# Optimization experiments

Measured on AMD Instinct MI355X. Metric: run time of the kernel, lower is better.

The kernel has to match this reference:

```python
import jax, jax.numpy as jnp
import numpy as np

M, K, E, N, TOPK = 4096, 1024, 8, 1024, 2

def setup_inputs() -> dict:
    key = jax.random.key(0)
    k1, k2, k3, k4, k5 = jax.random.split(key, 5)
    hidden_states = jax.random.normal(k1, (M, K), dtype=jnp.float32)
    w1 = jax.random.normal(k2, (E, K, 2 * N), dtype=jnp.float32) * 0.02
    w2 = jax.random.normal(k3, (E, N, K), dtype=jnp.float32) * 0.02
    topk_weights = jax.random.uniform(k4, (M, TOPK), dtype=jnp.float32)
    topk_ids = jax.random.randint(k5, (M, TOPK), 0, E, dtype=jnp.int64)
    return {"hidden_states": hidden_states, "w1": w1, "w2": w2,
            "topk_weights": topk_weights, "topk_ids": topk_ids}

def reference(hidden_states, w1, w2, topk_weights, topk_ids):
    # Fused MoE: per expert e, y_e = silu_and_mul(x @ w1[e]) @ w2[e];
    # output[m] = sum_k topk_weights[m,k] * y_{topk_ids[m,k]}[m]
    num_experts = w1.shape[0]
    n = w2.shape[1]

    def expert_step(acc, inputs):
        w1_e, w2_e, e = inputs
        gate_up = hidden_states @ w1_e            # [M, 2N]
        gate, up = gate_up[:, :n], gate_up[:, n:]
        h = jax.nn.silu(gate) * up                 # [M, N]
        y_e = h @ w2_e                             # [M, K]
        # combined routing weight of expert e per token (scatter-free finalize)
        coef = jnp.sum(jnp.where(topk_ids == e, topk_weights, 0.0), axis=1)  # [M]
        return acc + coef[:, None] * y_e, None

    init = jnp.zeros_like(hidden_states)
    out, _ = jax.lax.scan(expert_step, init,
                          (w1, w2, jnp.arange(num_experts, dtype=topk_ids.dtype)))
    return out
```

## Files before the change

kernel.cpp:

```cpp
#include <hip/hip_runtime.h>


#define M_TOK   4096
#define K_DIM   1024
#define N_DIM   1024
#define E_NUM   8
#define NPAIR   8192
#define BM      64
#define ROWS_CAP 8704
#define NROWBLK 136
#define HBLK    32

typedef unsigned short u16;
typedef unsigned int   u32;
typedef __attribute__((ext_vector_type(8))) short bf16x8;
typedef __attribute__((ext_vector_type(4))) float f32x4;

#define GPTR(p) ((const __attribute__((address_space(1))) u32*)(const void*)(p))
#define LPTR(p) ((__attribute__((address_space(3))) u32*)(void*)(p))

__device__ __forceinline__ u16 f2bf(float f) {
  union { float f; u32 u; } v; v.f = f;
  u32 r = v.u + 0x7FFFu + ((v.u >> 16) & 1u);
  return (u16)(r >> 16);
}
__device__ __forceinline__ float bf2f(u16 u) {
  union { u32 u; float f; } v; v.u = ((u32)u) << 16;
  return v.f;
}

__global__ __launch_bounds__(256) void hist_kernel(
    const int* __restrict__ topk_ids, int* __restrict__ blockhist) {
  __shared__ int wcnt[4][E_NUM];
  const int t = threadIdx.x, wave = t >> 6, lane = t & 63;
  int e = topk_ids[blockIdx.x * 256 + t] & 7;
#pragma unroll
  for (int ee = 0; ee < E_NUM; ++ee) {
    unsigned long long m = __ballot(e == ee);
    if (lane == ee) wcnt[wave][ee] = (int)__popcll(m);
  }
  __syncthreads();
  if (t < E_NUM) {
    int s = wcnt[0][t] + wcnt[1][t] + wcnt[2][t] + wcnt[3][t];
    blockhist[blockIdx.x * E_NUM + t] = s;
  }
}

__global__ __launch_bounds__(256) void scan_kernel(
    const int* __restrict__ blockhist, int* __restrict__ baseoff,
    int* __restrict__ pair_token, int* __restrict__ block_expert) {
  __shared__ int cnt[E_NUM], off[E_NUM], pad[E_NUM];
  const int t = threadIdx.x;
  if (t < E_NUM) {
    int run = 0;
    for (int b = 0; b < HBLK; ++b) {
      baseoff[b * E_NUM + t] = run;
      run += blockhist[b * E_NUM + t];
    }
    cnt[t] = run;
  }
  __syncthreads();
  if (t == 0) {
    int run = 0, blk = 0;
    for (int e = 0; e < E_NUM; ++e) {
      off[e] = run;
      int padded = ((cnt[e] + BM - 1) / BM) * BM;
      pad[e] = padded;
      for (int b = 0; b < padded / BM; ++b) block_expert[blk++] = e;
      run += padded;
    }
    for (; blk < NROWBLK; ++blk) block_expert[blk] = -1;
  }
  __syncthreads();
  for (int i = t; i < HBLK * E_NUM; i += 256) baseoff[i] += off[i & 7];
  for (int e = 0; e < E_NUM; ++e) {
    int s = off[e] + cnt[e], epos = off[e] + pad[e];
    for (int r = s + t; r < epos; r += 256) pair_token[r] = 0;
  }
}

__global__ __launch_bounds__(256) void assign_kernel(
    const int* __restrict__ topk_ids, const int* __restrict__ baseoff,
    int* __restrict__ pair_token, int* __restrict__ pos_of) {
  __shared__ int wcnt[4][E_NUM], wbase[4][E_NUM];
  const int t = threadIdx.x, wave = t >> 6, lane = t & 63;
  const int p = blockIdx.x * 256 + t;
  const int e = topk_ids[p] & 7;
  int rank = 0;
#pragma unroll
  for (int ee = 0; ee < E_NUM; ++ee) {
    unsigned long long m = __ballot(e == ee);
    if (e == ee) rank = (int)__popcll(m & ((1ull << lane) - 1ull));
    if (lane == ee) wcnt[wave][ee] = (int)__popcll(m);
  }
  __syncthreads();
  if (t < E_NUM) {
    int run = baseoff[blockIdx.x * E_NUM + t];
    for (int w = 0; w < 4; ++w) { wbase[w][t] = run; run += wcnt[w][t]; }
  }
  __syncthreads();
  int pos = wbase[wave][e] + rank;
  pair_token[pos] = p >> 1;
  pos_of[p] = pos;
}

__global__ __launch_bounds__(256) void convert_kernel(
    const float* __restrict__ in, u16* __restrict__ out) {
  int i = blockIdx.x * 256 + threadIdx.x;
  float4 v = ((const float4*)in)[i];
  ushort4 o;
  o.x = f2bf(v.x); o.y = f2bf(v.y); o.z = f2bf(v.z); o.w = f2bf(v.w);
  ((ushort4*)out)[i] = o;
}

__global__ __launch_bounds__(256) void transpose_convert(
    const float* __restrict__ in, u16* __restrict__ out, int R, int Cc) {
  __shared__ float lds[64][65];
  const float* src = in + (size_t)blockIdx.z * R * Cc;
  u16* dst = out + (size_t)blockIdx.z * R * Cc;
  int r0 = blockIdx.x * 64, c0 = blockIdx.y * 64;
  int t = threadIdx.x;
#pragma unroll
  for (int it = 0; it < 16; ++it) {
    int lin = it * 256 + t;
    int rr = lin >> 6, cc = lin & 63;
    lds[cc][rr] = src[(size_t)(r0 + rr) * Cc + c0 + cc];
  }
  __syncthreads();
#pragma unroll
  for (int it = 0; it < 8; ++it) {
    int lin = it * 512 + t * 2;
    int cc = lin >> 6, rr = lin & 63;
    ushort2 o;
    o.x = f2bf(lds[cc][rr]);
    o.y = f2bf(lds[cc][rr + 1]);
    *(ushort2*)&dst[(size_t)(c0 + cc) * R + r0 + rr] = o;
  }
}

template <bool GATHER, int NB>
__global__ __launch_bounds__(256, NB == 2 ? 3 : 4) void gemm64(
    const u16* __restrict__ A, const u16* __restrict__ Bt, u16* __restrict__ Out,
    const int* __restrict__ pair_token, const int* __restrict__ block_expert) {
  const int e = block_expert[blockIdx.x];
  if (e < 0) return;
  __shared__ __align__(16) u16 As[64 * 64];
  __shared__ __align__(16) u16 Bs[NB * 128 * 64];
  const int tid = threadIdx.x;
  const int wave = tid >> 6;
  const int lane = tid & 63;
  const int srow = wave * 8 + (lane >> 3);
  const int kc = ((lane & 7) ^ (srow & 7)) << 3;

  const u16* ap[2];
#pragma unroll
  for (int is = 0; is < 2; ++is) {
    int rt = is * 32 + srow;
    int grow = blockIdx.x * BM + rt;
    int arow = GATHER ? pair_token[grow] : grow;
    ap[is] = A + (size_t)arow * K_DIM + kc;
  }
  const u16* bp[NB][4];
  const u16* base_e = Bt + (size_t)e * (NB * N_DIM) * K_DIM;
#pragma unroll
  for (int nb = 0; nb < NB; ++nb)
#pragma unroll
    for (int is = 0; is < 4; ++is) {
      int rt = is * 32 + srow;
      int n = nb * N_DIM + blockIdx.y * 128 + rt;
      bp[nb][is] = base_e + (size_t)n * K_DIM + kc;
    }
  u16* alds = As + wave * 512;
  u16* blds = Bs + wave * 512;

  f32x4 acc[NB][4][2];
#pragma unroll
  for (int nb = 0; nb < NB; ++nb)
#pragma unroll
    for (int i = 0; i < 4; ++i)
#pragma unroll
      for (int j = 0; j < 2; ++j) acc[nb][i][j] = f32x4{0.f, 0.f, 0.f, 0.f};

  for (int k0 = 0; k0 < K_DIM; k0 += 64) {
#pragma unroll
    for (int is = 0; is < 2; ++is)
      __builtin_amdgcn_global_load_lds(GPTR(ap[is] + k0), LPTR(alds + is * 2048), 16, 0, 0);
#pragma unroll
    for (int nb = 0; nb < NB; ++nb)
#pragma unroll
      for (int is = 0; is < 4; ++is)
        __builtin_amdgcn_global_load_lds(GPTR(bp[nb][is] + k0), LPTR(blds + nb * 8192 + is * 2048), 16, 0, 0);
    __syncthreads();
#pragma unroll
    for (int ks = 0; ks < 2; ++ks) {
      const int cq = ks * 4 + (lane >> 4);
      bf16x8 af[4], bfr[NB][2];
#pragma unroll
      for (int i = 0; i < 4; ++i) {
        int row = i * 16 + (lane & 15);
        af[i] = *(const bf16x8*)&As[row * 64 + ((cq ^ (row & 7)) << 3)];
      }
#pragma unroll
      for (int nb = 0; nb < NB; ++nb)
#pragma unroll
        for (int j = 0; j < 2; ++j) {
          int n = wave * 32 + j * 16 + (lane & 15);
          bfr[nb][j] = *(const bf16x8*)&Bs[nb * 8192 + n * 64 + ((cq ^ (n & 7)) << 3)];
        }
#pragma unroll
      for (int nb = 0; nb < NB; ++nb)
#pragma unroll
        for (int i = 0; i < 4; ++i)
#pragma unroll
          for (int j = 0; j < 2; ++j)
            acc[nb][i][j] = __builtin_amdgcn_mfma_f32_16x16x32_bf16(af[i], bfr[nb][j], acc[nb][i][j], 0, 0, 0);
    }
    __syncthreads();
  }

  const size_t rbase = (size_t)blockIdx.x * BM + ((lane >> 4) * 4);
  const int cbase = blockIdx.y * 128 + wave * 32 + (lane & 15);
#pragma unroll
  for (int i = 0; i < 4; ++i)
#pragma unroll
    for (int j = 0; j < 2; ++j)
#pragma unroll
      for (int r = 0; r < 4; ++r) {
        float v;
        if (NB == 2) {
          float g = acc[0][i][j][r], u = acc[1][i][j][r];
          v = g * u / (1.f + __expf(-g));
        } else {
          v = acc[0][i][j][r];
        }
        Out[(rbase + i * 16 + r) * N_DIM + cbase + j * 16] = f2bf(v);
      }
}

__global__ __launch_bounds__(256) void gather_kernel(
    const u16* __restrict__ y, const float* __restrict__ tw,
    const int* __restrict__ pos_of, float* __restrict__ out) {
  int m = blockIdx.x;
  int k = threadIdx.x * 4;
  int p0 = pos_of[m * 2 + 0], p1 = pos_of[m * 2 + 1];
  float w0 = tw[m * 2 + 0], w1 = tw[m * 2 + 1];
  ushort4 y0 = *(const ushort4*)&y[(size_t)p0 * 1024 + k];
  ushort4 y1 = *(const ushort4*)&y[(size_t)p1 * 1024 + k];
  float4 o;
  o.x = w0 * bf2f(y0.x) + w1 * bf2f(y1.x);
  o.y = w0 * bf2f(y0.y) + w1 * bf2f(y1.y);
  o.z = w0 * bf2f(y0.z) + w1 * bf2f(y1.z);
  o.w = w0 * bf2f(y0.w) + w1 * bf2f(y1.w);
  *(float4*)&out[(size_t)m * 1024 + k] = o;
}

extern "C" void kernel_launch(void* const* d_in, const int* in_sizes, int n_in,
                              void* d_out, int out_size, void* d_ws, size_t ws_size,
                              hipStream_t stream) {
  const float* hs = (const float*)d_in[0];
  const float* w1 = (const float*)d_in[1];
  const float* w2 = (const float*)d_in[2];
  const float* tw = (const float*)d_in[3];
  const int* tids = (const int*)d_in[4];
  float* out = (float*)d_out;

  char* ws = (char*)d_ws;
  u16* hsb = (u16*)(ws);
  u16* w1t = (u16*)(ws + (size_t)(8u << 20));
  u16* w2t = (u16*)(ws + (size_t)(40u << 20));
  u16* h   = (u16*)(ws + (size_t)(56u << 20));
  u16* y   = (u16*)(ws + (size_t)(76u << 20));
  int* pair_token   = (int*)(ws + (size_t)(96u << 20));
  int* pos_of       = (int*)(ws + (size_t)(96u << 20) + 64 * 1024);
  int* block_expert = (int*)(ws + (size_t)(96u << 20) + 128 * 1024);
  int* blockhist    = (int*)(ws + (size_t)(96u << 20) + 192 * 1024);
  int* baseoff      = (int*)(ws + (size_t)(96u << 20) + 256 * 1024);

  hist_kernel<<<HBLK, 256, 0, stream>>>(tids, blockhist);
  scan_kernel<<<1, 256, 0, stream>>>(blockhist, baseoff, pair_token, block_expert);
  assign_kernel<<<HBLK, 256, 0, stream>>>(tids, baseoff, pair_token, pos_of);
  convert_kernel<<<4096, 256, 0, stream>>>(hs, hsb);
  transpose_convert<<<dim3(16, 32, E_NUM), 256, 0, stream>>>(w1, w1t, 1024, 2048);
  transpose_convert<<<dim3(16, 16, E_NUM), 256, 0, stream>>>(w2, w2t, 1024, 1024);
  gemm64<true, 2><<<dim3(NROWBLK, 8), 256, 0, stream>>>(hsb, w1t, h, pair_token, block_expert);
  gemm64<false, 1><<<dim3(NROWBLK, 8), 256, 0, stream>>>(h, w2t, y, pair_token, block_expert);
  gather_kernel<<<4096, 256, 0, stream>>>(y, tw, pos_of, out);
}
```

Before: 264.0 us.

## Fuse prep kernels and software-pipeline expert GEMMs with register-held B tiles

Merges the hidden-state conversion, both weight transpose-converts and the routing histogram into one launch to cut launch overhead and idle gaps. Rewrites the grouped GEMM as a double-buffered pipeline. A tiles stream into LDS via global_load_lds two steps ahead, while B fragments are loaded straight from global memory into registers and prefetched ahead, so B no longer goes through LDS. It also flattens the grid so the eight column blocks of one row block run adjacently, which should improve expert weight reuse in cache. The trade-off is higher register pressure (lower occupancy hints) and uncoalesced per-lane B loads.

```diff
diff --git a/kernel.cpp b/kernel.cpp
--- a/kernel.cpp
+++ b/kernel.cpp
@@ -10,6 +10,7 @@
 #define ROWS_CAP 8704
 #define NROWBLK 136
 #define HBLK    32
+#define NK      16
 
 typedef unsigned short u16;
 typedef unsigned int   u32;
@@ -29,20 +30,63 @@
   return v.f;
 }
 
-__global__ __launch_bounds__(256) void hist_kernel(
-    const int* __restrict__ topk_ids, int* __restrict__ blockhist) {
+__device__ __forceinline__ void transpose_body(
+    const float* __restrict__ in, u16* __restrict__ out, int R, int Cc,
+    int xt, int yt, int zt, float (*lds)[65]) {
+  const float* src = in + (size_t)zt * R * Cc;
+  u16* dst = out + (size_t)zt * R * Cc;
+  int r0 = xt * 64, c0 = yt * 64;
+  int t = threadIdx.x;
+#pragma unroll
+  for (int it = 0; it < 16; ++it) {
+    int lin = it * 256 + t;
+    int rr = lin >> 6, cc = lin & 63;
+    lds[cc][rr] = src[(size_t)(r0 + rr) * Cc + c0 + cc];
+  }
+  __syncthreads();
+#pragma unroll
+  for (int it = 0; it < 8; ++it) {
+    int lin = it * 512 + t * 2;
+    int cc = lin >> 6, rr = lin & 63;
+    ushort2 o;
+    o.x = f2bf(lds[cc][rr]);
+    o.y = f2bf(lds[cc][rr + 1]);
+    *(ushort2*)&dst[(size_t)(c0 + cc) * R + r0 + rr] = o;
+  }
+}
+
+__global__ __launch_bounds__(256) void prep_kernel(
+    const float* __restrict__ hs, const float* __restrict__ w1,
+    const float* __restrict__ w2, const int* __restrict__ topk_ids,
+    u16* __restrict__ hsb, u16* __restrict__ w1t, u16* __restrict__ w2t,
+    int* __restrict__ blockhist) {
+  __shared__ float tlds[64][65];
   __shared__ int wcnt[4][E_NUM];
-  const int t = threadIdx.x, wave = t >> 6, lane = t & 63;
-  int e = topk_ids[blockIdx.x * 256 + t] & 7;
-#pragma unroll
-  for (int ee = 0; ee < E_NUM; ++ee) {
-    unsigned long long m = __ballot(e == ee);
-    if (lane == ee) wcnt[wave][ee] = (int)__popcll(m);
-  }
-  __syncthreads();
-  if (t < E_NUM) {
-    int s = wcnt[0][t] + wcnt[1][t] + wcnt[2][t] + wcnt[3][t];
-    blockhist[blockIdx.x * E_NUM + t] = s;
+  const int b = blockIdx.x, t = threadIdx.x;
+  if (b < 4096) {
+    int i = b * 256 + t;
+    float4 v = ((const float4*)hs)[i];
+    ushort4 o;
+    o.x = f2bf(v.x); o.y = f2bf(v.y); o.z = f2bf(v.z); o.w = f2bf(v.w);
+    ((ushort4*)hsb)[i] = o;
+  } else if (b < 8192) {
+    int idx = b - 4096;
+    transpose_body(w1, w1t, 1024, 2048, idx & 15, (idx >> 4) & 31, idx >> 9, tlds);
+  } else if (b < 10240) {
+    int idx = b - 8192;
+    transpose_body(w2, w2t, 1024, 1024, idx & 15, (idx >> 4) & 15, idx >> 8, tlds);
+  } else {
+    int blk = b - 10240;
+    const int wave = t >> 6, lane = t & 63;
+    int e = topk_ids[blk * 256 + t] & 7;
+#pragma unroll
+    for (int ee = 0; ee < E_NUM; ++ee) {
+      unsigned long long m = __ballot(e == ee);
+      if (lane == ee) wcnt[wave][ee] = (int)__popcll(m);
+    }
+    __syncthreads();
+    if (t < E_NUM)
+      blockhist[blk * E_NUM + t] = wcnt[0][t] + wcnt[1][t] + wcnt[2][t] + wcnt[3][t];
   }
 }
 
@@ -104,48 +148,46 @@
   pos_of[p] = pos;
 }
 
-__global__ __launch_bounds__(256) void convert_kernel(
-    const float* __restrict__ in, u16* __restrict__ out) {
-  int i = blockIdx.x * 256 + threadIdx.x;
-  float4 v = ((const float4*)in)[i];
-  ushort4 o;
-  o.x = f2bf(v.x); o.y = f2bf(v.y); o.z = f2bf(v.z); o.w = f2bf(v.w);
-  ((ushort4*)out)[i] = o;
-}
-
-__global__ __launch_bounds__(256) void transpose_convert(
-    const float* __restrict__ in, u16* __restrict__ out, int R, int Cc) {
-  __shared__ float lds[64][65];
-  const float* src = in + (size_t)blockIdx.z * R * Cc;
-  u16* dst = out + (size_t)blockIdx.z * R * Cc;
-  int r0 = blockIdx.x * 64, c0 = blockIdx.y * 64;
-  int t = threadIdx.x;
-#pragma unroll
-  for (int it = 0; it < 16; ++it) {
-    int lin = it * 256 + t;
-    int rr = lin >> 6, cc = lin & 63;
-    lds[cc][rr] = src[(size_t)(r0 + rr) * Cc + c0 + cc];
-  }
-  __syncthreads();
-#pragma unroll
-  for (int it = 0; it < 8; ++it) {
-    int lin = it * 512 + t * 2;
-    int cc = lin >> 6, rr = lin & 63;
-    ushort2 o;
-    o.x = f2bf(lds[cc][rr]);
-    o.y = f2bf(lds[cc][rr + 1]);
-    *(ushort2*)&dst[(size_t)(c0 + cc) * R + r0 + rr] = o;
-  }
-}
-
-template <bool GATHER, int NB>
-__global__ __launch_bounds__(256, NB == 2 ? 3 : 4) void gemm64(
+#define STEP(it, cur)                                                          \
+  {                                                                            \
+    bf16x8 afr[2][4];                                                          \
+    _Pragma("unroll") for (int ks = 0; ks < 2; ++ks)                           \
+      _Pragma("unroll") for (int i = 0; i < 4; ++i) {                          \
+        int row = i * 16 + (lane & 15);                                        \
+        int cq = ks * 4 + (lane >> 4);                                         \
+        afr[ks][i] = *(const bf16x8*)&As[(cur) * 4096 + row * 64 +             \
+                                         ((cq ^ (row & 7)) << 3)];             \
+      }                                                                        \
+    __syncthreads();                                                           \
+    if ((it) + 2 < NK) {                                                       \
+      _Pragma("unroll") for (int is = 0; is < 2; ++is)                         \
+        __builtin_amdgcn_global_load_lds(GPTR(ap[is] + (it) * 64 + 128),       \
+            LPTR(As + (cur) * 4096 + wave * 512 + is * 2048), 16, 0, 0);       \
+    }                                                                          \
+    _Pragma("unroll") for (int ks = 0; ks < 2; ++ks)                           \
+      _Pragma("unroll") for (int nb = 0; nb < NB; ++nb)                        \
+        _Pragma("unroll") for (int i = 0; i < 4; ++i)                          \
+          _Pragma("unroll") for (int j = 0; j < 2; ++j)                        \
+            acc[nb][i][j] = __builtin_amdgcn_mfma_f32_16x16x32_bf16(           \
+                afr[ks][i], breg[cur][nb][j][ks], acc[nb][i][j], 0, 0, 0);     \
+    if ((it) + 2 < NK) {                                                       \
+      _Pragma("unroll") for (int nb = 0; nb < NB; ++nb)                        \
+        _Pragma("unroll") for (int j = 0; j < 2; ++j)                          \
+          _Pragma("unroll") for (int ks = 0; ks < 2; ++ks)                     \
+            breg[cur][nb][j][ks] =                                             \
+                *(const bf16x8*)(bq[nb][j] + (it) * 64 + 128 + ks * 32);       \
+    }                                                                          \
+  }
+
+template <bool GATHER, int NB, int MINW>
+__global__ __launch_bounds__(256, MINW) void gemm_pl(
     const u16* __restrict__ A, const u16* __restrict__ Bt, u16* __restrict__ Out,
     const int* __restrict__ pair_token, const int* __restrict__ block_expert) {
-  const int e = block_expert[blockIdx.x];
+  const int by = blockIdx.x & 7;
+  const int rbk = blockIdx.x >> 3;
+  const int e = block_expert[rbk];
   if (e < 0) return;
-  __shared__ __align__(16) u16 As[64 * 64];
-  __shared__ __align__(16) u16 Bs[NB * 128 * 64];
+  __shared__ __align__(16) u16 As[2 * 4096];
   const int tid = threadIdx.x;
   const int wave = tid >> 6;
   const int lane = tid & 63;
@@ -156,22 +198,19 @@
 #pragma unroll
   for (int is = 0; is < 2; ++is) {
     int rt = is * 32 + srow;
-    int grow = blockIdx.x * BM + rt;
+    int grow = rbk * BM + rt;
     int arow = GATHER ? pair_token[grow] : grow;
     ap[is] = A + (size_t)arow * K_DIM + kc;
   }
-  const u16* bp[NB][4];
+  const u16* bq[NB][2];
   const u16* base_e = Bt + (size_t)e * (NB * N_DIM) * K_DIM;
 #pragma unroll
   for (int nb = 0; nb < NB; ++nb)
 #pragma unroll
-    for (int is = 0; is < 4; ++is) {
-      int rt = is * 32 + srow;
-      int n = nb * N_DIM + blockIdx.y * 128 + rt;
-      bp[nb][is] = base_e + (size_t)n * K_DIM + kc;
+    for (int j = 0; j < 2; ++j) {
+      int n = nb * N_DIM + by * 128 + wave * 32 + j * 16 + (lane & 15);
+      bq[nb][j] = base_e + (size_t)n * K_DIM + ((lane >> 4) << 3);
     }
-  u16* alds = As + wave * 512;
-  u16* blds = Bs + wave * 512;
 
   f32x4 acc[NB][4][2];
 #pragma unroll
@@ -181,45 +220,31 @@
 #pragma unroll
       for (int j = 0; j < 2; ++j) acc[nb][i][j] = f32x4{0.f, 0.f, 0.f, 0.f};
 
-  for (int k0 = 0; k0 < K_DIM; k0 += 64) {
-#pragma unroll
-    for (int is = 0; is < 2; ++is)
-      __builtin_amdgcn_global_load_lds(GPTR(ap[is] + k0), LPTR(alds + is * 2048), 16, 0, 0);
-#pragma unroll
-    for (int nb = 0; nb < NB; ++nb)
-#pragma unroll
-      for (int is = 0; is < 4; ++is)
-        __builtin_amdgcn_global_load_lds(GPTR(bp[nb][is] + k0), LPTR(blds + nb * 8192 + is * 2048), 16, 0, 0);
-    __syncthreads();
-#pragma unroll
-    for (int ks = 0; ks < 2; ++ks) {
-      const int cq = ks * 4 + (lane >> 4);
-      bf16x8 af[4], bfr[NB][2];
-#pragma unroll
-      for (int i = 0; i < 4; ++i) {
-        int row = i * 16 + (lane & 15);
-        af[i] = *(const bf16x8*)&As[row * 64 + ((cq ^ (row & 7)) << 3)];
+  bf16x8 breg[2][NB][2][2];
+#pragma unroll
+  for (int is = 0; is < 2; ++is)
+    __builtin_amdgcn_global_load_lds(GPTR(ap[is]), LPTR(As + wave * 512 + is * 2048), 16, 0, 0);
+#pragma unroll
+  for (int is = 0; is < 2; ++is)
+    __builtin_amdgcn_global_load_lds(GPTR(ap[is] + 64), LPTR(As + 4096 + wave * 512 + is * 2048), 16, 0, 0);
+#pragma unroll
+  for (int nb = 0; nb < NB; ++nb)
+#pragma unroll
+    for (int j = 0; j < 2; ++j)
+#pragma unroll
+      for (int ks = 0; ks < 2; ++ks) {
+        breg[0][nb][j][ks] = *(const bf16x8*)(bq[nb][j] + ks * 32);
+        breg[1][nb][j][ks] = *(const bf16x8*)(bq[nb][j] + 64 + ks * 32);
       }
-#pragma unroll
-      for (int nb = 0; nb < NB; ++nb)
-#pragma unroll
-        for (int j = 0; j < 2; ++j) {
-          int n = wave * 32 + j * 16 + (lane & 15);
-          bfr[nb][j] = *(const bf16x8*)&Bs[nb * 8192 + n * 64 + ((cq ^ (n & 7)) << 3)];
-        }
-#pragma unroll
-      for (int nb = 0; nb < NB; ++nb)
-#pragma unroll
-        for (int i = 0; i < 4; ++i)
-#pragma unroll
-          for (int j = 0; j < 2; ++j)
-            acc[nb][i][j] = __builtin_amdgcn_mfma_f32_16x16x32_bf16(af[i], bfr[nb][j], acc[nb][i][j], 0, 0, 0);
-    }
-    __syncthreads();
-  }
-
-  const size_t rbase = (size_t)blockIdx.x * BM + ((lane >> 4) * 4);
-  const int cbase = blockIdx.y * 128 + wave * 32 + (lane & 15);
+  __syncthreads();
+
+  for (int it = 0; it < NK; it += 2) {
+    STEP(it, 0);
+    STEP(it + 1, 1);
+  }
+
+  const size_t rbase = (size_t)rbk * BM + ((lane >> 4) * 4);
+  const int cbase = by * 128 + wave * 32 + (lane & 15);
 #pragma unroll
   for (int i = 0; i < 4; ++i)
 #pragma unroll
@@ -276,13 +301,10 @@
   int* blockhist    = (int*)(ws + (size_t)(96u << 20) + 192 * 1024);
   int* baseoff      = (int*)(ws + (size_t)(96u << 20) + 256 * 1024);
 
-  hist_kernel<<<HBLK, 256, 0, stream>>>(tids, blockhist);
+  prep_kernel<<<10240 + HBLK, 256, 0, stream>>>(hs, w1, w2, tids, hsb, w1t, w2t, blockhist);
   scan_kernel<<<1, 256, 0, stream>>>(blockhist, baseoff, pair_token, block_expert);
   assign_kernel<<<HBLK, 256, 0, stream>>>(tids, baseoff, pair_token, pos_of);
-  convert_kernel<<<4096, 256, 0, stream>>>(hs, hsb);
-  transpose_convert<<<dim3(16, 32, E_NUM), 256, 0, stream>>>(w1, w1t, 1024, 2048);
-  transpose_convert<<<dim3(16, 16, E_NUM), 256, 0, stream>>>(w2, w2t, 1024, 1024);
-  gemm64<true, 2><<<dim3(NROWBLK, 8), 256, 0, stream>>>(hsb, w1t, h, pair_token, block_expert);
-  gemm64<false, 1><<<dim3(NROWBLK, 8), 256, 0, stream>>>(h, w2t, y, pair_token, block_expert);
+  gemm_pl<true, 2, 2><<<NROWBLK * 8, 256, 0, stream>>>(hsb, w1t, h, pair_token, block_expert);
+  gemm_pl<false, 1, 3><<<NROWBLK * 8, 256, 0, stream>>>(h, w2t, y, pair_token, block_expert);
   gather_kernel<<<4096, 256, 0, stream>>>(y, tw, pos_of, out);
 }
```

Result: slower. 299.6 us (+13.5%).
